# Performance work log

Hardware: AMD Instinct MI355X
Metric: run time of the kernel (lower is better)

Reference implementation:

```python
import jax, jax.numpy as jnp
import numpy as np

B, N, K, D = 256, 64, 12, 128


def setup_inputs() -> dict:
    key = jax.random.key(0)
    ks = jax.random.split(key, 12)
    s = 1.0 / np.sqrt(D)
    inp = {
        "nodes_hidden": jax.random.normal(ks[0], (B, N, D), jnp.float32),
        "neighbors_hidden": jax.random.normal(ks[1], (B, N, K, D), jnp.float32),
        # binary neighbor-validity mask (float, as in the torch code)
        "mask": (jax.random.uniform(ks[2], (B, N, K)) < 0.7).astype(jnp.float32),
        "Wq": jax.random.uniform(ks[3], (D, D), jnp.float32, -s, s),
        "bq": jax.random.uniform(ks[4], (D,), jnp.float32, -s, s),
        "Wk": jax.random.uniform(ks[5], (D, D), jnp.float32, -s, s),
        "bk": jax.random.uniform(ks[6], (D,), jnp.float32, -s, s),
        "Wv": jax.random.uniform(ks[7], (D, D), jnp.float32, -s, s),
        "bv": jax.random.uniform(ks[8], (D,), jnp.float32, -s, s),
        # W_att: Linear(2D -> 1); split into the query half and key half of its weight
        "wa_q": jax.random.uniform(ks[9], (D,), jnp.float32, -s, s),
        "wa_k": jax.random.uniform(ks[10], (D,), jnp.float32, -s, s),
        "ba": jax.random.uniform(ks[11], (), jnp.float32, -s, s),
    }
    return inp


def reference(nodes_hidden, neighbors_hidden, mask, Wq, bq, Wk, bk, Wv, bv, wa_q, wa_k, ba):
    # prepend the node itself to its neighbor list: [B,N,K+1,D]
    nh = jnp.concatenate([nodes_hidden[:, :, None, :], neighbors_hidden], axis=2)
    # prepend an always-valid slot to the mask: [B,N,K+1]
    m = jnp.concatenate([jnp.ones(mask.shape[:-1] + (1,), mask.dtype), mask], axis=-1)

    q = nodes_hidden @ Wq + bq            # [B,N,D]
    k = nh @ Wk + bk                      # [B,N,K+1,D]
    v = nh @ Wv + bv                      # [B,N,K+1,D]

    # W_att(cat([q,k])) == q.wa_q + k.wa_k + ba  (avoids materializing the 2D concat)
    sim = (q @ wa_q)[:, :, None] + k @ wa_k + ba   # [B,N,K+1]
    sim = jnp.where(sim >= 0, sim, 0.2 * sim)      # LeakyReLU(0.2)
    sim = jnp.exp(sim) * m                         # masked exp (matches torch exactly)
    attn = sim / (jnp.sum(sim, axis=-1, keepdims=True) + 1e-16)
    return jnp.einsum('bnk,bnkd->bnd', attn, v)    # [B,N,D]
```

## Files before the change

### kernel.cpp

```cpp
#include <hip/hip_runtime.h>


#define B_  256
#define N_  64
#define K_  12
#define D_  128
#define BN  (B_ * N_)
#define ROWS 16
#define HB_STRIDE 132

#define PIN4(v)  asm volatile("" : "+v"(v.x), "+v"(v.y), "+v"(v.z), "+v"(v.w))
#define PIN1(s)  asm volatile("" : "+v"(s))

__global__ void prep_kernel(const float* __restrict__ Wq, const float* __restrict__ bq,
                            const float* __restrict__ Wk, const float* __restrict__ bk,
                            const float* __restrict__ wa_q, const float* __restrict__ wa_k,
                            float* __restrict__ ws) {
    int g = blockIdx.x;
    int l = threadIdx.x;
    const float* row;
    const float* wa;
    float* outp;
    if (g < 128)      { row = Wq + g * D_;         wa = wa_q; outp = ws + g; }
    else if (g < 256) { row = Wk + (g - 128) * D_; wa = wa_k; outp = ws + 128 + (g - 128); }
    else if (g == 256){ row = bq;                  wa = wa_q; outp = ws + 256; }
    else              { row = bk;                  wa = wa_k; outp = ws + 257; }

    float2 r = ((const float2*)row)[l];
    float2 w = ((const float2*)wa)[l];
    float p = r.x * w.x + r.y * w.y;
    #pragma unroll
    for (int m = 1; m < 64; m <<= 1) p += __shfl_xor(p, m, 64);
    if (l == 0) *outp = p;
}

__global__ void __launch_bounds__(256, 4)
fused_kernel(const float* __restrict__ nodes, const float* __restrict__ neigh,
             const float* __restrict__ mask, const float* __restrict__ ba_p,
             const float* __restrict__ ws, const float* __restrict__ Wv,
             const float* __restrict__ bv, float* __restrict__ out) {
    __shared__ float hb[ROWS * HB_STRIDE];
    __shared__ float scL[ROWS];

    const int t    = threadIdx.x;
    const int wave = t >> 6;
    const int l    = t & 63;
    const int li   = l & 31;
    const int h    = l >> 5;
    const int j8   = l & 7;

    const float cq  = ws[256];
    const float ckb = ws[257];
    const float ba  = ba_p[0];
    const float cst = cq + ckb + ba;
    const float4 wqe4 = ((const float4*)ws)[li];
    const float4 wke4 = ((const float4*)(ws + 128))[li];

    const int idx0 = blockIdx.x * ROWS + wave * 4;

    float4 xb[2][6];
    float4 nv[2];
    float  mv[2];

    #define LOADP(buf, pi) do {                                              \
        const int idx_ = idx0 + (pi);                                        \
        nv[buf] = ((const float4*)(nodes + (size_t)idx_ * D_))[li];          \
        const float4* gp_ = (const float4*)(neigh + (size_t)idx_ * (K_*D_)); \
        xb[buf][0] = gp_[0 * 64 + l];                                        \
        xb[buf][1] = gp_[1 * 64 + l];                                        \
        xb[buf][2] = gp_[2 * 64 + l];                                        \
        xb[buf][3] = gp_[3 * 64 + l];                                        \
        xb[buf][4] = gp_[4 * 64 + l];                                        \
        xb[buf][5] = gp_[5 * 64 + l];                                        \
        mv[buf] = (j8 < 6) ? mask[(size_t)idx_ * K_ + 2 * j8 + h] : 0.0f;    \
    } while (0)

    LOADP(0, 0);

    #pragma unroll
    for (int i = 0; i < 4; ++i) {
        const int b  = i & 1;
        const int nb = b ^ 1;
        if (i < 3) LOADP(nb, i + 1);
        __builtin_amdgcn_sched_barrier(0);

        float v[8];
        v[7] = nv[b].x*wqe4.x + nv[b].y*wqe4.y + nv[b].z*wqe4.z + nv[b].w*wqe4.w;
        v[6] = nv[b].x*wke4.x + nv[b].y*wke4.y + nv[b].z*wke4.z + nv[b].w*wke4.w;
        #pragma unroll
        for (int q = 0; q < 6; ++q)
            v[q] = xb[b][q].x*wke4.x + xb[b][q].y*wke4.y
                 + xb[b][q].z*wke4.z + xb[b][q].w*wke4.w;

        PIN4(xb[b][0]); PIN4(xb[b][1]); PIN4(xb[b][2]);
        PIN4(xb[b][3]); PIN4(xb[b][4]); PIN4(xb[b][5]);
        PIN4(nv[b]);    PIN1(mv[b]);

        float A0, A1, A2, A3;
        {
            const bool hi = (l & 1);
            float g0 = hi ? v[0] : v[1];
            float g1 = hi ? v[2] : v[3];
            float g2 = hi ? v[4] : v[5];
            float g3 = hi ? v[6] : v[7];
            g0 = __shfl_xor(g0, 1, 64);
            g1 = __shfl_xor(g1, 1, 64);
            g2 = __shfl_xor(g2, 1, 64);
            g3 = __shfl_xor(g3, 1, 64);
            A0 = (hi ? v[1] : v[0]) + g0;
            A1 = (hi ? v[3] : v[2]) + g1;
            A2 = (hi ? v[5] : v[4]) + g2;
            A3 = (hi ? v[7] : v[6]) + g3;
        }
        float B0, B1;
        {
            const bool hi = (l & 2);
            float g0 = hi ? A0 : A1;
            float g1 = hi ? A2 : A3;
            g0 = __shfl_xor(g0, 2, 64);
            g1 = __shfl_xor(g1, 2, 64);
            B0 = (hi ? A1 : A0) + g0;
            B1 = (hi ? A3 : A2) + g1;
        }
        float c;
        {
            const bool hi = (l & 4);
            float g = hi ? B0 : B1;
            g = __shfl_xor(g, 4, 64);
            c = (hi ? B1 : B0) + g;
        }
        c += __shfl_xor(c, 8, 64);
        c += __shfl_xor(c, 16, 64);

        const float pq  = __shfl(c, 7, 8);
        const float pkn = __shfl(c, 6, 8);
        const float base = pq + cst;

        float s0 = base + pkn;
        s0 = (s0 >= 0.0f) ? s0 : 0.2f * s0;
        const float e0 = __expf(s0);
        float sj = base + c;
        sj = (sj >= 0.0f) ? sj : 0.2f * sj;
        const float ej = (j8 < 6) ? __expf(sj) * mv[b] : 0.0f;

        const float an = (h == 0) ? e0 : 0.0f;
        float4 acc;
        acc.x = an * nv[b].x;
        acc.y = an * nv[b].y;
        acc.z = an * nv[b].z;
        acc.w = an * nv[b].w;
        float Se = 0.0f;
        #pragma unroll
        for (int q = 0; q < 6; ++q) {
            const float bi = __shfl(ej, q, 8);
            acc.x += bi * xb[b][q].x;
            acc.y += bi * xb[b][q].y;
            acc.z += bi * xb[b][q].z;
            acc.w += bi * xb[b][q].w;
            Se    += bi;
        }
        acc.x += __shfl_xor(acc.x, 32, 64);
        acc.y += __shfl_xor(acc.y, 32, 64);
        acc.z += __shfl_xor(acc.z, 32, 64);
        acc.w += __shfl_xor(acc.w, 32, 64);
        Se    += __shfl_xor(Se,    32, 64);

        const float S   = e0 + Se;
        const float inv = 1.0f / (S + 1e-16f);
        if (h == 0) {
            const int lrow = wave * 4 + i;
            float4 o;
            o.x = acc.x * inv;
            o.y = acc.y * inv;
            o.z = acc.z * inv;
            o.w = acc.w * inv;
            *(float4*)(hb + lrow * HB_STRIDE + 4 * li) = o;
            if (li == 0) scL[lrow] = S * inv;
        }
    }
    #undef LOADP
    __syncthreads();

    const int rg = t >> 5;
    const int cg = t & 31;
    const float4* wv4 = (const float4*)Wv;
    const float* hr0 = hb + rg * HB_STRIDE;
    const float* hr1 = hb + (rg + 8) * HB_STRIDE;

    float4 acc0 = make_float4(0.0f, 0.0f, 0.0f, 0.0f);
    float4 acc1 = make_float4(0.0f, 0.0f, 0.0f, 0.0f);
    #pragma unroll 8
    for (int kq = 0; kq < 32; ++kq) {
        const float4 a0 = *(const float4*)(hr0 + 4 * kq);
        const float4 a1 = *(const float4*)(hr1 + 4 * kq);
        #pragma unroll
        for (int e = 0; e < 4; ++e) {
            const float4 w = wv4[(4 * kq + e) * 32 + cg];
            const float f0 = (e == 0) ? a0.x : (e == 1) ? a0.y : (e == 2) ? a0.z : a0.w;
            const float f1 = (e == 0) ? a1.x : (e == 1) ? a1.y : (e == 2) ? a1.z : a1.w;
            acc0.x += f0 * w.x; acc0.y += f0 * w.y;
            acc0.z += f0 * w.z; acc0.w += f0 * w.w;
            acc1.x += f1 * w.x; acc1.y += f1 * w.y;
            acc1.z += f1 * w.z; acc1.w += f1 * w.w;
        }
    }

    const float4 bvv = ((const float4*)bv)[cg];
    const int row0 = blockIdx.x * ROWS;
    {
        const float s = scL[rg];
        float4 o;
        o.x = acc0.x + bvv.x * s;
        o.y = acc0.y + bvv.y * s;
        o.z = acc0.z + bvv.z * s;
        o.w = acc0.w + bvv.w * s;
        *(float4*)(out + (size_t)(row0 + rg) * D_ + cg * 4) = o;
    }
    {
        const float s = scL[rg + 8];
        float4 o;
        o.x = acc1.x + bvv.x * s;
        o.y = acc1.y + bvv.y * s;
        o.z = acc1.z + bvv.z * s;
        o.w = acc1.w + bvv.w * s;
        *(float4*)(out + (size_t)(row0 + rg + 8) * D_ + cg * 4) = o;
    }
}

extern "C" void kernel_launch(void* const* d_in, const int* in_sizes, int n_in,
                              void* d_out, int out_size, void* d_ws, size_t ws_size,
                              hipStream_t stream) {
    const float* nodes = (const float*)d_in[0];
    const float* neigh = (const float*)d_in[1];
    const float* mask  = (const float*)d_in[2];
    const float* Wq    = (const float*)d_in[3];
    const float* bq    = (const float*)d_in[4];
    const float* Wk    = (const float*)d_in[5];
    const float* bk    = (const float*)d_in[6];
    const float* Wv    = (const float*)d_in[7];
    const float* bv    = (const float*)d_in[8];
    const float* wa_q  = (const float*)d_in[9];
    const float* wa_k  = (const float*)d_in[10];
    const float* ba    = (const float*)d_in[11];
    float* out = (float*)d_out;
    float* ws  = (float*)d_ws;

    prep_kernel<<<258, 64, 0, stream>>>(Wq, bq, Wk, bk, wa_q, wa_k, ws);
    fused_kernel<<<BN / ROWS, 256, 0, stream>>>(nodes, neigh, mask, ba, ws, Wv, bv, out);
}
```

Baseline: 188.8 us.

## Stage neighbor tiles through LDS with async global_load_lds double buffering

New measurement: 191.6 us. About the same (+1.5%).

```diff
diff --git a/kernel.cpp b/kernel.cpp
--- a/kernel.cpp
+++ b/kernel.cpp
@@ -6,11 +6,10 @@
 #define K_  12
 #define D_  128
 #define BN  (B_ * N_)
-#define ROWS 16
+#define TP    4
+#define TILES 4
+#define ROWS  16
 #define HB_STRIDE 132
-
-#define PIN4(v)  asm volatile("" : "+v"(v.x), "+v"(v.y), "+v"(v.z), "+v"(v.w))
-#define PIN1(s)  asm volatile("" : "+v"(s))
 
 __global__ void prep_kernel(const float* __restrict__ Wq, const float* __restrict__ bq,
                             const float* __restrict__ Wk, const float* __restrict__ bk,
@@ -34,11 +33,20 @@
     if (l == 0) *outp = p;
 }
 
-__global__ void __launch_bounds__(256, 4)
+__device__ __forceinline__ void gll16(const float* g, float* l) {
+    __builtin_amdgcn_global_load_lds(
+        (const __attribute__((address_space(1))) unsigned int*)g,
+        (__attribute__((address_space(3))) unsigned int*)l, 16, 0, 0);
+}
+
+__global__ void __launch_bounds__(256)
 fused_kernel(const float* __restrict__ nodes, const float* __restrict__ neigh,
              const float* __restrict__ mask, const float* __restrict__ ba_p,
              const float* __restrict__ ws, const float* __restrict__ Wv,
              const float* __restrict__ bv, float* __restrict__ out) {
+    __shared__ float nb[2][TP * K_ * D_];
+    __shared__ float ndb[2][TP * D_];
+    __shared__ float mb[2][TP * K_];
     __shared__ float hb[ROWS * HB_STRIDE];
     __shared__ float scL[ROWS];
 
@@ -56,130 +64,126 @@
     const float4 wqe4 = ((const float4*)ws)[li];
     const float4 wke4 = ((const float4*)(ws + 128))[li];
 
-    const int idx0 = blockIdx.x * ROWS + wave * 4;
-
-    float4 xb[2][6];
-    float4 nv[2];
-    float  mv[2];
-
-    #define LOADP(buf, pi) do {                                              \
-        const int idx_ = idx0 + (pi);                                        \
-        nv[buf] = ((const float4*)(nodes + (size_t)idx_ * D_))[li];          \
-        const float4* gp_ = (const float4*)(neigh + (size_t)idx_ * (K_*D_)); \
-        xb[buf][0] = gp_[0 * 64 + l];                                        \
-        xb[buf][1] = gp_[1 * 64 + l];                                        \
-        xb[buf][2] = gp_[2 * 64 + l];                                        \
-        xb[buf][3] = gp_[3 * 64 + l];                                        \
-        xb[buf][4] = gp_[4 * 64 + l];                                        \
-        xb[buf][5] = gp_[5 * 64 + l];                                        \
-        mv[buf] = (j8 < 6) ? mask[(size_t)idx_ * K_ + 2 * j8 + h] : 0.0f;    \
+    const int base_pair = blockIdx.x * ROWS;
+
+    #define STAGE(buf, tt) do {                                               \
+        const int tb_ = base_pair + (tt) * TP;                                \
+        const float* ns_ = neigh + (size_t)tb_ * (K_ * D_);                   \
+        _Pragma("unroll")                                                     \
+        for (int i_ = 0; i_ < 6; ++i_)                                        \
+            gll16(ns_ + i_ * 1024 + t * 4, &nb[buf][i_ * 1024 + t * 4]);      \
+        if (wave < 2)                                                         \
+            gll16(nodes + (size_t)tb_ * D_ + t * 4, &ndb[buf][t * 4]);        \
+        else if (wave == 2 && l < 12)                                         \
+            gll16(mask + (size_t)tb_ * K_ + l * 4, &mb[buf][l * 4]);          \
     } while (0)
 
-    LOADP(0, 0);
-
+    #define COMPUTE(buf, tt) do {                                             \
+        const float* nbp_ = &nb[buf][wave * (K_ * D_)];                       \
+        const float* ndp_ = &ndb[buf][wave * D_];                             \
+        const float4 nv_ = *(const float4*)(ndp_ + 4 * li);                   \
+        float4 x0_ = *(const float4*)(nbp_ + (0 + h) * D_ + 4 * li);          \
+        float4 x1_ = *(const float4*)(nbp_ + (2 + h) * D_ + 4 * li);          \
+        float4 x2_ = *(const float4*)(nbp_ + (4 + h) * D_ + 4 * li);          \
+        float4 x3_ = *(const float4*)(nbp_ + (6 + h) * D_ + 4 * li);          \
+        float4 x4_ = *(const float4*)(nbp_ + (8 + h) * D_ + 4 * li);          \
+        float4 x5_ = *(const float4*)(nbp_ + (10 + h) * D_ + 4 * li);         \
+        float v0 = x0_.x*wke4.x + x0_.y*wke4.y + x0_.z*wke4.z + x0_.w*wke4.w; \
+        float v1 = x1_.x*wke4.x + x1_.y*wke4.y + x1_.z*wke4.z + x1_.w*wke4.w; \
+        float v2 = x2_.x*wke4.x + x2_.y*wke4.y + x2_.z*wke4.z + x2_.w*wke4.w; \
+        float v3 = x3_.x*wke4.x + x3_.y*wke4.y + x3_.z*wke4.z + x3_.w*wke4.w; \
+        float v4 = x4_.x*wke4.x + x4_.y*wke4.y + x4_.z*wke4.z + x4_.w*wke4.w; \
+        float v5 = x5_.x*wke4.x + x5_.y*wke4.y + x5_.z*wke4.z + x5_.w*wke4.w; \
+        float v6 = nv_.x*wke4.x + nv_.y*wke4.y + nv_.z*wke4.z + nv_.w*wke4.w; \
+        float v7 = nv_.x*wqe4.x + nv_.y*wqe4.y + nv_.z*wqe4.z + nv_.w*wqe4.w; \
+        float A0, A1, A2, A3;                                                 \
+        {                                                                     \
+            const bool hi_ = (l & 1);                                         \
+            float g0 = __shfl_xor(hi_ ? v0 : v1, 1, 64);                      \
+            float g1 = __shfl_xor(hi_ ? v2 : v3, 1, 64);                      \
+            float g2 = __shfl_xor(hi_ ? v4 : v5, 1, 64);                      \
+            float g3 = __shfl_xor(hi_ ? v6 : v7, 1, 64);                      \
+            A0 = (hi_ ? v1 : v0) + g0;                                        \
+            A1 = (hi_ ? v3 : v2) + g1;                                        \
+            A2 = (hi_ ? v5 : v4) + g2;                                        \
+            A3 = (hi_ ? v7 : v6) + g3;                                        \
+        }                                                                     \
+        float B0, B1;                                                         \
+        {                                                                     \
+            const bool hi_ = (l & 2);                                         \
+            float g0 = __shfl_xor(hi_ ? A0 : A1, 2, 64);                      \
+            float g1 = __shfl_xor(hi_ ? A2 : A3, 2, 64);                      \
+            B0 = (hi_ ? A1 : A0) + g0;                                        \
+            B1 = (hi_ ? A3 : A2) + g1;                                        \
+        }                                                                     \
+        float c;                                                              \
+        {                                                                     \
+            const bool hi_ = (l & 4);                                         \
+            float g = __shfl_xor(hi_ ? B0 : B1, 4, 64);                       \
+            c = (hi_ ? B1 : B0) + g;                                          \
+        }                                                                     \
+        c += __shfl_xor(c, 8, 64);                                            \
+        c += __shfl_xor(c, 16, 64);                                           \
+        const float pq_  = __shfl(c, 7, 8);                                   \
+        const float pkn_ = __shfl(c, 6, 8);                                   \
+        const float base_ = pq_ + cst;                                        \
+        float s0_ = base_ + pkn_;                                             \
+        s0_ = (s0_ >= 0.0f) ? s0_ : 0.2f * s0_;                               \
+        const float e0_ = __expf(s0_);                                        \
+        float sj_ = base_ + c;                                                \
+        sj_ = (sj_ >= 0.0f) ? sj_ : 0.2f * sj_;                               \
+        float ej_ = 0.0f;                                                     \
+        if (j8 < 6) ej_ = __expf(sj_) * mb[buf][wave * K_ + 2 * j8 + h];      \
+        const float an_ = (h == 0) ? e0_ : 0.0f;                              \
+        float ax = an_ * nv_.x, ay = an_ * nv_.y;                             \
+        float az = an_ * nv_.z, aw = an_ * nv_.w;                             \
+        float Se_ = 0.0f;                                                     \
+        {                                                                     \
+            float bi_;                                                        \
+            bi_ = __shfl(ej_, 0, 8); Se_ += bi_;                              \
+            ax += bi_*x0_.x; ay += bi_*x0_.y; az += bi_*x0_.z; aw += bi_*x0_.w; \
+            bi_ = __shfl(ej_, 1, 8); Se_ += bi_;                              \
+            ax += bi_*x1_.x; ay += bi_*x1_.y; az += bi_*x1_.z; aw += bi_*x1_.w; \
+            bi_ = __shfl(ej_, 2, 8); Se_ += bi_;                              \
+            ax += bi_*x2_.x; ay += bi_*x2_.y; az += bi_*x2_.z; aw += bi_*x2_.w; \
+            bi_ = __shfl(ej_, 3, 8); Se_ += bi_;                              \
+            ax += bi_*x3_.x; ay += bi_*x3_.y; az += bi_*x3_.z; aw += bi_*x3_.w; \
+            bi_ = __shfl(ej_, 4, 8); Se_ += bi_;                              \
+            ax += bi_*x4_.x; ay += bi_*x4_.y; az += bi_*x4_.z; aw += bi_*x4_.w; \
+            bi_ = __shfl(ej_, 5, 8); Se_ += bi_;                              \
+            ax += bi_*x5_.x; ay += bi_*x5_.y; az += bi_*x5_.z; aw += bi_*x5_.w; \
+        }                                                                     \
+        ax += __shfl_xor(ax, 32, 64);                                         \
+        ay += __shfl_xor(ay, 32, 64);                                         \
+        az += __shfl_xor(az, 32, 64);                                         \
+        aw += __shfl_xor(aw, 32, 64);                                         \
+        Se_ += __shfl_xor(Se_, 32, 64);                                       \
+        const float S_   = e0_ + Se_;                                         \
+        const float inv_ = 1.0f / (S_ + 1e-16f);                              \
+        if (h == 0) {                                                         \
+            const int lrow_ = (tt) * TP + wave;                               \
+            float4 o_;                                                        \
+            o_.x = ax * inv_;                                                 \
+            o_.y = ay * inv_;                                                 \
+            o_.z = az * inv_;                                                 \
+            o_.w = aw * inv_;                                                 \
+            *(float4*)(hb + lrow_ * HB_STRIDE + 4 * li) = o_;                 \
+            if (li == 0) scL[lrow_] = S_ * inv_;                              \
+        }                                                                     \
+    } while (0)
+
+    STAGE(0, 0);
+    __syncthreads();
     #pragma unroll
-    for (int i = 0; i < 4; ++i) {
-        const int b  = i & 1;
-        const int nb = b ^ 1;
-        if (i < 3) LOADP(nb, i + 1);
+    for (int tt = 0; tt < TILES; ++tt) {
+        const int cur = tt & 1;
+        if (tt + 1 < TILES) STAGE((tt + 1) & 1, tt + 1);
         __builtin_amdgcn_sched_barrier(0);
-
-        float v[8];
-        v[7] = nv[b].x*wqe4.x + nv[b].y*wqe4.y + nv[b].z*wqe4.z + nv[b].w*wqe4.w;
-        v[6] = nv[b].x*wke4.x + nv[b].y*wke4.y + nv[b].z*wke4.z + nv[b].w*wke4.w;
-        #pragma unroll
-        for (int q = 0; q < 6; ++q)
-            v[q] = xb[b][q].x*wke4.x + xb[b][q].y*wke4.y
-                 + xb[b][q].z*wke4.z + xb[b][q].w*wke4.w;
-
-        PIN4(xb[b][0]); PIN4(xb[b][1]); PIN4(xb[b][2]);
-        PIN4(xb[b][3]); PIN4(xb[b][4]); PIN4(xb[b][5]);
-        PIN4(nv[b]);    PIN1(mv[b]);
-
-        float A0, A1, A2, A3;
-        {
-            const bool hi = (l & 1);
-            float g0 = hi ? v[0] : v[1];
-            float g1 = hi ? v[2] : v[3];
-            float g2 = hi ? v[4] : v[5];
-            float g3 = hi ? v[6] : v[7];
-            g0 = __shfl_xor(g0, 1, 64);
-            g1 = __shfl_xor(g1, 1, 64);
-            g2 = __shfl_xor(g2, 1, 64);
-            g3 = __shfl_xor(g3, 1, 64);
-            A0 = (hi ? v[1] : v[0]) + g0;
-            A1 = (hi ? v[3] : v[2]) + g1;
-            A2 = (hi ? v[5] : v[4]) + g2;
-            A3 = (hi ? v[7] : v[6]) + g3;
-        }
-        float B0, B1;
-        {
-            const bool hi = (l & 2);
-            float g0 = hi ? A0 : A1;
-            float g1 = hi ? A2 : A3;
-            g0 = __shfl_xor(g0, 2, 64);
-            g1 = __shfl_xor(g1, 2, 64);
-            B0 = (hi ? A1 : A0) + g0;
-            B1 = (hi ? A3 : A2) + g1;
-        }
-        float c;
-        {
-            const bool hi = (l & 4);
-            float g = hi ? B0 : B1;
-            g = __shfl_xor(g, 4, 64);
-            c = (hi ? B1 : B0) + g;
-        }
-        c += __shfl_xor(c, 8, 64);
-        c += __shfl_xor(c, 16, 64);
-
-        const float pq  = __shfl(c, 7, 8);
-        const float pkn = __shfl(c, 6, 8);
-        const float base = pq + cst;
-
-        float s0 = base + pkn;
-        s0 = (s0 >= 0.0f) ? s0 : 0.2f * s0;
-        const float e0 = __expf(s0);
-        float sj = base + c;
-        sj = (sj >= 0.0f) ? sj : 0.2f * sj;
-        const float ej = (j8 < 6) ? __expf(sj) * mv[b] : 0.0f;
-
-        const float an = (h == 0) ? e0 : 0.0f;
-        float4 acc;
-        acc.x = an * nv[b].x;
-        acc.y = an * nv[b].y;
-        acc.z = an * nv[b].z;
-        acc.w = an * nv[b].w;
-        float Se = 0.0f;
-        #pragma unroll
-        for (int q = 0; q < 6; ++q) {
-            const float bi = __shfl(ej, q, 8);
-            acc.x += bi * xb[b][q].x;
-            acc.y += bi * xb[b][q].y;
-            acc.z += bi * xb[b][q].z;
-            acc.w += bi * xb[b][q].w;
-            Se    += bi;
-        }
-        acc.x += __shfl_xor(acc.x, 32, 64);
-        acc.y += __shfl_xor(acc.y, 32, 64);
-        acc.z += __shfl_xor(acc.z, 32, 64);
-        acc.w += __shfl_xor(acc.w, 32, 64);
-        Se    += __shfl_xor(Se,    32, 64);
-
-        const float S   = e0 + Se;
-        const float inv = 1.0f / (S + 1e-16f);
-        if (h == 0) {
-            const int lrow = wave * 4 + i;
-            float4 o;
-            o.x = acc.x * inv;
-            o.y = acc.y * inv;
-            o.z = acc.z * inv;
-            o.w = acc.w * inv;
-            *(float4*)(hb + lrow * HB_STRIDE + 4 * li) = o;
-            if (li == 0) scL[lrow] = S * inv;
-        }
-    }
-    #undef LOADP
-    __syncthreads();
+        COMPUTE(cur, tt);
+        __syncthreads();
+    }
+    #undef STAGE
+    #undef COMPUTE
 
     const int rg = t >> 5;
     const int cg = t & 31;
@@ -206,7 +210,6 @@
     }
 
     const float4 bvv = ((const float4*)bv)[cg];
-    const int row0 = blockIdx.x * ROWS;
     {
         const float s = scL[rg];
         float4 o;
@@ -214,7 +217,7 @@
         o.y = acc0.y + bvv.y * s;
         o.z = acc0.z + bvv.z * s;
         o.w = acc0.w + bvv.w * s;
-        *(float4*)(out + (size_t)(row0 + rg) * D_ + cg * 4) = o;
+        *(float4*)(out + (size_t)(base_pair + rg) * D_ + cg * 4) = o;
     }
     {
         const float s = scL[rg + 8];
@@ -223,7 +226,7 @@
         o.y = acc1.y + bvv.y * s;
         o.z = acc1.z + bvv.z * s;
         o.w = acc1.w + bvv.w * s;
-        *(float4*)(out + (size_t)(row0 + rg + 8) * D_ + cg * 4) = o;
+        *(float4*)(out + (size_t)(base_pair + rg + 8) * D_ + cg * 4) = o;
     }
 }
 
```
